# Kernel optimization log

Hardware: AMD Instinct MI355X
Metric: run time of the kernel (lower is better)

## Reference

```python
import jax, jax.numpy as jnp
import numpy as np

B, S, D, K = 4, 8192, 512, 20


def setup_inputs() -> dict:
    key = jax.random.key(0)
    k1, k2, k3, k4 = jax.random.split(key, 4)
    std = 0.02  # _init_weights: normal(0, 0.02/sqrt(layer_idx+1)), layer_idx=0
    return {
        "x": jax.random.normal(k1, (B, S, D), dtype=jnp.float32),
        "positions": jax.random.normal(k2, (K, D), dtype=jnp.float32) * 0.2,
        "log_scales": jnp.log(1.0 + 0.5 * jax.random.uniform(k3, (K,), dtype=jnp.float32)),
        "amplitudes": 1.2 + 0.3 * jax.random.uniform(k4, (K,), dtype=jnp.float32),
        "w_v": jax.random.normal(jax.random.fold_in(key, 10), (D, D), dtype=jnp.float32) * std,
        "w_o": jax.random.normal(jax.random.fold_in(key, 11), (D, D), dtype=jnp.float32) * std,
    }


def reference(x, positions, log_scales, amplitudes, w_v, w_o):
    # Gaussian-splat RBF attention (token -> splat -> token routing).
    scales = jnp.exp(log_scales)  # [K]
    # squared distances ||x - c||^2 via expansion (avoids [B,S,K,D] tensor)
    x2 = jnp.sum(x * x, axis=-1, keepdims=True)           # [B,S,1]
    c2 = jnp.sum(positions * positions, axis=-1)          # [K]
    xc = jnp.einsum('bsd,kd->bsk', x, positions)          # [B,S,K]
    d2 = jnp.maximum(x2 - 2.0 * xc + c2, 0.0)             # [B,S,K]
    gauss = amplitudes * jnp.exp(-0.5 * d2 / (scales * scales))  # [B,S,K]
    attn = gauss / (jnp.sum(gauss, axis=-1, keepdims=True) + 1e-8)  # per-token normalize
    v = jnp.einsum('bsd,ed->bse', x, w_v)                 # token_value_proj (no bias)
    splat_states = jnp.einsum('bsk,bsd->bkd', attn, v)    # gather token values at splats
    out = jnp.einsum('bsk,bkd->bsd', attn, splat_states)  # scatter back to tokens
    return jnp.einsum('bsd,ed->bse', out, w_o)            # output_proj (dropout=eval identity)
```

## Files before the change

### kernel.cpp

```cpp
#include <hip/hip_runtime.h>
#include <hip/hip_bf16.h>

#define BB 4
#define SS 8192
#define DD 512
#define KK 20
#define CHUNKS 64

__global__ void k0_params(const float* __restrict__ pos,
                          const float* __restrict__ log_scales,
                          const float* __restrict__ amps,
                          float* __restrict__ params) {
  int k = blockIdx.x;
  int lane = threadIdx.x;
  float acc = 0.f;
  for (int d = lane; d < DD; d += 64) { float p = pos[k * DD + d]; acc += p * p; }
#pragma unroll
  for (int off = 32; off > 0; off >>= 1) acc += __shfl_xor(acc, off);
  if (lane == 0) {
    params[k] = acc;
    float s = __expf(log_scales[k]);
    params[KK + k] = 0.5f / (s * s);
    params[2 * KK + k] = amps[k];
  }
}

__global__ __launch_bounds__(256) void k1_attn(
    const float* __restrict__ x, const float* __restrict__ pos,
    const float* __restrict__ params, float* __restrict__ attn) {
  __shared__ float pos_s[KK * DD];
  int tid = threadIdx.x;
  for (int i = tid; i < KK * DD / 4; i += 256)
    ((float4*)pos_s)[i] = ((const float4*)pos)[i];
  __syncthreads();

  int tl = tid >> 2;
  int dsub = tid & 3;
  size_t tok = (size_t)blockIdx.x * 64 + tl;
  const float* xrow = x + tok * DD;

  float acc[KK];
#pragma unroll
  for (int k = 0; k < KK; ++k) acc[k] = 0.f;
  float x2 = 0.f;

#pragma unroll 4
  for (int j = 0; j < 32; ++j) {
    int d0 = j * 16 + dsub * 4;
    float4 xv = *(const float4*)(xrow + d0);
    x2 += xv.x * xv.x + xv.y * xv.y + xv.z * xv.z + xv.w * xv.w;
#pragma unroll
    for (int k = 0; k < KK; ++k) {
      float4 p = *(const float4*)(pos_s + k * DD + d0);
      acc[k] += xv.x * p.x + xv.y * p.y + xv.z * p.z + xv.w * p.w;
    }
  }
#pragma unroll
  for (int k = 0; k < KK; ++k) {
    acc[k] += __shfl_xor(acc[k], 1);
    acc[k] += __shfl_xor(acc[k], 2);
  }
  x2 += __shfl_xor(x2, 1);
  x2 += __shfl_xor(x2, 2);

  if (dsub == 0) {
    float g[KK];
    float sum = 0.f;
#pragma unroll
    for (int k = 0; k < KK; ++k) {
      float d2 = fmaxf(x2 - 2.f * acc[k] + params[k], 0.f);
      float gk = params[2 * KK + k] * __expf(-params[KK + k] * d2);
      g[k] = gk;
      sum += gk;
    }
    float inv = 1.f / (sum + 1e-8f);
    float* arow = attn + tok * KK;
#pragma unroll
    for (int k = 0; k < KK; ++k) arow[k] = g[k] * inv;
  }
}

__global__ __launch_bounds__(256) void k2_scatter(
    const float* __restrict__ x, const float* __restrict__ attn,
    float* __restrict__ Mpart) {
  int t = threadIdx.x;
  int c = blockIdx.x;
  int b = blockIdx.y;
  int s0 = c * (SS / CHUNKS);

  float2 Ml[KK];
#pragma unroll
  for (int k = 0; k < KK; ++k) Ml[k] = make_float2(0.f, 0.f);

  for (int s = s0; s < s0 + SS / CHUNKS; ++s) {
    size_t tokb = (size_t)b * SS + s;
    float2 xv = *(const float2*)(x + tokb * DD + 2 * t);
    const float* arow = attn + tokb * KK;
#pragma unroll
    for (int k = 0; k < KK; ++k) {
      float a = arow[k];
      Ml[k].x += a * xv.x;
      Ml[k].y += a * xv.y;
    }
  }
  float* base = Mpart + (((size_t)b * CHUNKS + c) * KK) * DD + 2 * t;
#pragma unroll
  for (int k = 0; k < KK; ++k)
    *(float2*)(base + (size_t)k * DD) = Ml[k];
}

__global__ __launch_bounds__(256) void k2b_reduce(
    const float* __restrict__ Mpart, float* __restrict__ Mg) {
  int idx = blockIdx.x * 256 + threadIdx.x;
  int b = idx / (KK * DD);
  int kd = idx - b * (KK * DD);
  const float* p = Mpart + (size_t)b * CHUNKS * KK * DD + kd;
  float acc = 0.f;
#pragma unroll 8
  for (int c = 0; c < CHUNKS; ++c) acc += p[(size_t)c * KK * DD];
  Mg[idx] = acc;
}

__global__ __launch_bounds__(256) void k3_proj(
    const float* __restrict__ in, const float* __restrict__ W,
    float* __restrict__ out) {
  __shared__ float row_s[DD];
  int bk = blockIdx.x;
  int t = threadIdx.x;
  for (int i = t; i < DD / 4; i += 256)
    ((float4*)row_s)[i] = ((const float4*)(in + (size_t)bk * DD))[i];
  __syncthreads();
  int e = blockIdx.y * 256 + t;
  const float* wrow = W + (size_t)e * DD;
  float acc = 0.f;
#pragma unroll 4
  for (int j = 0; j < DD / 4; ++j) {
    float4 w4 = *(const float4*)(wrow + 4 * j);
    float4 m4 = ((const float4*)row_s)[j];
    acc += m4.x * w4.x + m4.y * w4.y + m4.z * w4.z + m4.w * w4.w;
  }
  out[(size_t)bk * DD + e] = acc;
}

__global__ __launch_bounds__(256) void k5_gather(
    const float* __restrict__ attn, const float* __restrict__ ws2,
    float* __restrict__ out) {
  int t = threadIdx.x;
  int b = blockIdx.y;
  int s0 = blockIdx.x * (SS / CHUNKS);

  float2 w[KK];
#pragma unroll
  for (int k = 0; k < KK; ++k)
    w[k] = *(const float2*)(ws2 + ((size_t)b * KK + k) * DD + 2 * t);

  for (int s = s0; s < s0 + SS / CHUNKS; ++s) {
    size_t tokb = (size_t)b * SS + s;
    const float* arow = attn + tokb * KK;
    float2 o = make_float2(0.f, 0.f);
#pragma unroll
    for (int k = 0; k < KK; ++k) {
      float a = arow[k];
      o.x += a * w[k].x;
      o.y += a * w[k].y;
    }
    *(float2*)(out + tokb * DD + 2 * t) = o;
  }
}

extern "C" void kernel_launch(void* const* d_in, const int* in_sizes, int n_in,
                              void* d_out, int out_size, void* d_ws, size_t ws_size,
                              hipStream_t stream) {
  const float* x   = (const float*)d_in[0];
  const float* pos = (const float*)d_in[1];
  const float* ls  = (const float*)d_in[2];
  const float* am  = (const float*)d_in[3];
  const float* w_v = (const float*)d_in[4];
  const float* w_o = (const float*)d_in[5];
  float* out = (float*)d_out;

  float* ws     = (float*)d_ws;
  float* params = ws;
  float* attn   = ws + 64;
  float* Mg     = attn + (size_t)BB * SS * KK;
  float* ssb    = Mg + (size_t)BB * KK * DD;
  float* ws2    = ssb + (size_t)BB * KK * DD;
  float* Mpart  = ws2 + (size_t)BB * KK * DD;

  k0_params<<<KK, 64, 0, stream>>>(pos, ls, am, params);
  k1_attn<<<(BB * SS) / 64, 256, 0, stream>>>(x, pos, params, attn);
  k2_scatter<<<dim3(CHUNKS, BB), 256, 0, stream>>>(x, attn, Mpart);
  k2b_reduce<<<(BB * KK * DD) / 256, 256, 0, stream>>>(Mpart, Mg);
  k3_proj<<<dim3(BB * KK, 2), 256, 0, stream>>>(Mg, w_v, ssb);
  k3_proj<<<dim3(BB * KK, 2), 256, 0, stream>>>(ssb, w_o, ws2);
  k5_gather<<<dim3(CHUNKS, BB), 256, 0, stream>>>(attn, ws2, out);
}
```

Before: 250.6 us.

## Restructure splat attention kernels for more parallelism and fuse reduce with projections

Rewrites the attention kernel so each block handles 32 tokens, with two rows per 16-lane group. Positions are reused across both rows and the params are cached in shared memory. The scatter stage runs on many more chunks (256 per batch, or 128 if the workspace is too small) and reads attention rows as float4. The chunk reduction and both projections are fused into one 512-thread kernel. The gather stage uses float4 outputs across 2048 blocks. The aim is to raise occupancy on the bandwidth-bound scatter/gather stages and cut launches. The cost is a larger partial-sum buffer and a serial 256-way reduction inside the fused kernel.

Result: slower. 280.8 us (+12.0%).

```diff
diff --git a/kernel.cpp b/kernel.cpp
--- a/kernel.cpp
+++ b/kernel.cpp
@@ -5,7 +5,10 @@
 #define SS 8192
 #define DD 512
 #define KK 20
-#define CHUNKS 64
+
+__device__ __forceinline__ float dot4(float4 a, float4 b) {
+  return a.x * b.x + a.y * b.y + a.z * b.z + a.w * b.w;
+}
 
 __global__ void k0_params(const float* __restrict__ pos,
                           const float* __restrict__ log_scales,
@@ -25,146 +28,180 @@
   }
 }
 
-__global__ __launch_bounds__(256) void k1_attn(
+__global__ __launch_bounds__(256) void kA_attn(
     const float* __restrict__ x, const float* __restrict__ pos,
-    const float* __restrict__ params, float* __restrict__ attn) {
+    const float* __restrict__ params, float* __restrict__ attn_g) {
   __shared__ float pos_s[KK * DD];
+  __shared__ float prm_s[3 * KK];
   int tid = threadIdx.x;
   for (int i = tid; i < KK * DD / 4; i += 256)
     ((float4*)pos_s)[i] = ((const float4*)pos)[i];
+  if (tid < 3 * KK) prm_s[tid] = params[tid];
   __syncthreads();
 
-  int tl = tid >> 2;
-  int dsub = tid & 3;
-  size_t tok = (size_t)blockIdx.x * 64 + tl;
-  const float* xrow = x + tok * DD;
-
-  float acc[KK];
-#pragma unroll
-  for (int k = 0; k < KK; ++k) acc[k] = 0.f;
-  float x2 = 0.f;
-
-#pragma unroll 4
-  for (int j = 0; j < 32; ++j) {
-    int d0 = j * 16 + dsub * 4;
-    float4 xv = *(const float4*)(xrow + d0);
-    x2 += xv.x * xv.x + xv.y * xv.y + xv.z * xv.z + xv.w * xv.w;
+  int b = blockIdx.x >> 8;
+  int c = blockIdx.x & 255;
+  size_t row0 = (size_t)b * SS + (size_t)c * 32;
+  int g = tid >> 4;
+  int dsub = tid & 15;
+
+  const float* xA = x + (row0 + g) * DD;
+  const float* xB = xA + 16 * DD;
+
+  float accA[KK], accB[KK], x2A = 0.f, x2B = 0.f;
+#pragma unroll
+  for (int k = 0; k < KK; ++k) { accA[k] = 0.f; accB[k] = 0.f; }
+
+#pragma unroll 2
+  for (int j = 0; j < 8; ++j) {
+    int d0 = j * 64 + dsub * 4;
+    float4 xa = *(const float4*)(xA + d0);
+    float4 xb = *(const float4*)(xB + d0);
+    x2A += dot4(xa, xa);
+    x2B += dot4(xb, xb);
 #pragma unroll
     for (int k = 0; k < KK; ++k) {
       float4 p = *(const float4*)(pos_s + k * DD + d0);
-      acc[k] += xv.x * p.x + xv.y * p.y + xv.z * p.z + xv.w * p.w;
-    }
-  }
+      accA[k] += dot4(xa, p);
+      accB[k] += dot4(xb, p);
+    }
+  }
+
+#pragma unroll
+  for (int m = 1; m <= 8; m <<= 1) { x2A += __shfl_xor(x2A, m); x2B += __shfl_xor(x2B, m); }
 #pragma unroll
   for (int k = 0; k < KK; ++k) {
-    acc[k] += __shfl_xor(acc[k], 1);
-    acc[k] += __shfl_xor(acc[k], 2);
-  }
-  x2 += __shfl_xor(x2, 1);
-  x2 += __shfl_xor(x2, 2);
+#pragma unroll
+    for (int m = 1; m <= 8; m <<= 1) {
+      accA[k] += __shfl_xor(accA[k], m);
+      accB[k] += __shfl_xor(accB[k], m);
+    }
+  }
 
   if (dsub == 0) {
-    float g[KK];
+    float gg[KK];
     float sum = 0.f;
 #pragma unroll
     for (int k = 0; k < KK; ++k) {
-      float d2 = fmaxf(x2 - 2.f * acc[k] + params[k], 0.f);
-      float gk = params[2 * KK + k] * __expf(-params[KK + k] * d2);
-      g[k] = gk;
-      sum += gk;
+      float d2 = fmaxf(x2A - 2.f * accA[k] + prm_s[k], 0.f);
+      gg[k] = prm_s[2 * KK + k] * __expf(-prm_s[KK + k] * d2);
+      sum += gg[k];
     }
     float inv = 1.f / (sum + 1e-8f);
-    float* arow = attn + tok * KK;
-#pragma unroll
-    for (int k = 0; k < KK; ++k) arow[k] = g[k] * inv;
-  }
-}
-
-__global__ __launch_bounds__(256) void k2_scatter(
+    float* ar = attn_g + (row0 + g) * KK;
+#pragma unroll
+    for (int k = 0; k < KK; ++k) ar[k] = gg[k] * inv;
+
+    sum = 0.f;
+#pragma unroll
+    for (int k = 0; k < KK; ++k) {
+      float d2 = fmaxf(x2B - 2.f * accB[k] + prm_s[k], 0.f);
+      gg[k] = prm_s[2 * KK + k] * __expf(-prm_s[KK + k] * d2);
+      sum += gg[k];
+    }
+    inv = 1.f / (sum + 1e-8f);
+    ar = attn_g + (row0 + g + 16) * KK;
+#pragma unroll
+    for (int k = 0; k < KK; ++k) ar[k] = gg[k] * inv;
+  }
+}
+
+__global__ __launch_bounds__(256) void kB_scatter(
     const float* __restrict__ x, const float* __restrict__ attn,
-    float* __restrict__ Mpart) {
+    float* __restrict__ Mpart, int tpc) {
   int t = threadIdx.x;
   int c = blockIdx.x;
   int b = blockIdx.y;
-  int s0 = c * (SS / CHUNKS);
+  int cpb = gridDim.x;
+  size_t row0 = (size_t)b * SS + (size_t)c * tpc;
 
   float2 Ml[KK];
 #pragma unroll
   for (int k = 0; k < KK; ++k) Ml[k] = make_float2(0.f, 0.f);
 
-  for (int s = s0; s < s0 + SS / CHUNKS; ++s) {
-    size_t tokb = (size_t)b * SS + s;
-    float2 xv = *(const float2*)(x + tokb * DD + 2 * t);
-    const float* arow = attn + tokb * KK;
-#pragma unroll
-    for (int k = 0; k < KK; ++k) {
-      float a = arow[k];
-      Ml[k].x += a * xv.x;
-      Ml[k].y += a * xv.y;
-    }
-  }
-  float* base = Mpart + (((size_t)b * CHUNKS + c) * KK) * DD + 2 * t;
-#pragma unroll
-  for (int k = 0; k < KK; ++k)
-    *(float2*)(base + (size_t)k * DD) = Ml[k];
-}
-
-__global__ __launch_bounds__(256) void k2b_reduce(
-    const float* __restrict__ Mpart, float* __restrict__ Mg) {
-  int idx = blockIdx.x * 256 + threadIdx.x;
-  int b = idx / (KK * DD);
-  int kd = idx - b * (KK * DD);
-  const float* p = Mpart + (size_t)b * CHUNKS * KK * DD + kd;
+  const float* xb = x + row0 * DD + 2 * t;
+  const float* ab = attn + row0 * KK;
+  for (int s = 0; s < tpc; ++s) {
+    float2 xv = *(const float2*)(xb + (size_t)s * DD);
+    const float4* ar4 = (const float4*)(ab + s * KK);
+#pragma unroll
+    for (int kk = 0; kk < KK / 4; ++kk) {
+      float4 a4 = ar4[kk];
+      Ml[4 * kk + 0].x += a4.x * xv.x; Ml[4 * kk + 0].y += a4.x * xv.y;
+      Ml[4 * kk + 1].x += a4.y * xv.x; Ml[4 * kk + 1].y += a4.y * xv.y;
+      Ml[4 * kk + 2].x += a4.z * xv.x; Ml[4 * kk + 2].y += a4.z * xv.y;
+      Ml[4 * kk + 3].x += a4.w * xv.x; Ml[4 * kk + 3].y += a4.w * xv.y;
+    }
+  }
+  float* mp = Mpart + ((size_t)b * cpb + c) * KK * DD + 2 * t;
+#pragma unroll
+  for (int k = 0; k < KK; ++k) *(float2*)(mp + (size_t)k * DD) = Ml[k];
+}
+
+__global__ __launch_bounds__(512) void k3f(
+    const float* __restrict__ Mpart, const float* __restrict__ w_v,
+    const float* __restrict__ w_o, float* __restrict__ ws2, int cpb) {
+  __shared__ float m_s[DD];
+  __shared__ float v_s[DD];
+  int bk = blockIdx.x;
+  int b = bk / KK, k = bk - b * KK;
+  int e = threadIdx.x;
+
+  const float* mp = Mpart + ((size_t)b * cpb) * KK * DD + (size_t)k * DD + e;
   float acc = 0.f;
 #pragma unroll 8
-  for (int c = 0; c < CHUNKS; ++c) acc += p[(size_t)c * KK * DD];
-  Mg[idx] = acc;
-}
-
-__global__ __launch_bounds__(256) void k3_proj(
-    const float* __restrict__ in, const float* __restrict__ W,
-    float* __restrict__ out) {
-  __shared__ float row_s[DD];
-  int bk = blockIdx.x;
-  int t = threadIdx.x;
-  for (int i = t; i < DD / 4; i += 256)
-    ((float4*)row_s)[i] = ((const float4*)(in + (size_t)bk * DD))[i];
+  for (int c = 0; c < cpb; ++c) acc += mp[(size_t)c * KK * DD];
+  m_s[e] = acc;
   __syncthreads();
-  int e = blockIdx.y * 256 + t;
-  const float* wrow = W + (size_t)e * DD;
-  float acc = 0.f;
+
+  const float4* wr = (const float4*)(w_v + (size_t)e * DD);
+  float a2 = 0.f;
 #pragma unroll 4
-  for (int j = 0; j < DD / 4; ++j) {
-    float4 w4 = *(const float4*)(wrow + 4 * j);
-    float4 m4 = ((const float4*)row_s)[j];
-    acc += m4.x * w4.x + m4.y * w4.y + m4.z * w4.z + m4.w * w4.w;
-  }
-  out[(size_t)bk * DD + e] = acc;
+  for (int j = 0; j < DD / 4; ++j) a2 += dot4(((const float4*)m_s)[j], wr[j]);
+  v_s[e] = a2;
+  __syncthreads();
+
+  const float4* wr2 = (const float4*)(w_o + (size_t)e * DD);
+  float a3 = 0.f;
+#pragma unroll 4
+  for (int j = 0; j < DD / 4; ++j) a3 += dot4(((const float4*)v_s)[j], wr2[j]);
+  ws2[(size_t)bk * DD + e] = a3;
 }
 
 __global__ __launch_bounds__(256) void k5_gather(
     const float* __restrict__ attn, const float* __restrict__ ws2,
     float* __restrict__ out) {
-  int t = threadIdx.x;
-  int b = blockIdx.y;
-  int s0 = blockIdx.x * (SS / CHUNKS);
-
-  float2 w[KK];
-#pragma unroll
-  for (int k = 0; k < KK; ++k)
-    w[k] = *(const float2*)(ws2 + ((size_t)b * KK + k) * DD + 2 * t);
-
-  for (int s = s0; s < s0 + SS / CHUNKS; ++s) {
-    size_t tokb = (size_t)b * SS + s;
-    const float* arow = attn + tokb * KK;
-    float2 o = make_float2(0.f, 0.f);
-#pragma unroll
-    for (int k = 0; k < KK; ++k) {
-      float a = arow[k];
-      o.x += a * w[k].x;
-      o.y += a * w[k].y;
-    }
-    *(float2*)(out + tokb * DD + 2 * t) = o;
+  int tid = threadIdx.x;
+  int b = blockIdx.x >> 9;
+  int sc = blockIdx.x & 511;
+  size_t s0 = (size_t)sc * 16;
+  int tr = tid >> 7;
+  int e4 = tid & 127;
+
+  float4 w[KK];
+  const float* wb = ws2 + (size_t)b * KK * DD + e4 * 4;
+#pragma unroll
+  for (int k = 0; k < KK; ++k) w[k] = *(const float4*)(wb + (size_t)k * DD);
+
+  size_t rowA = (size_t)b * SS + s0 + tr;
+  const float* ar = attn + rowA * KK;
+  float* orow = out + rowA * DD + e4 * 4;
+
+#pragma unroll 2
+  for (int i = 0; i < 8; ++i) {
+    const float4* a4 = (const float4*)(ar + (size_t)2 * i * KK);
+    float4 A = a4[0], Bv = a4[1], C = a4[2], Dv = a4[3], E = a4[4];
+    float4 o = make_float4(0.f, 0.f, 0.f, 0.f);
+#define ACC(av, kbase) \
+    o.x += av * w[kbase].x; o.y += av * w[kbase].y; \
+    o.z += av * w[kbase].z; o.w += av * w[kbase].w;
+    ACC(A.x, 0)  ACC(A.y, 1)  ACC(A.z, 2)  ACC(A.w, 3)
+    ACC(Bv.x, 4) ACC(Bv.y, 5) ACC(Bv.z, 6) ACC(Bv.w, 7)
+    ACC(C.x, 8)  ACC(C.y, 9)  ACC(C.z, 10) ACC(C.w, 11)
+    ACC(Dv.x, 12) ACC(Dv.y, 13) ACC(Dv.z, 14) ACC(Dv.w, 15)
+    ACC(E.x, 16) ACC(E.y, 17) ACC(E.z, 18) ACC(E.w, 19)
+#undef ACC
+    *(float4*)(orow + (size_t)2 * i * DD) = o;
   }
 }
 
@@ -180,18 +217,19 @@
   float* out = (float*)d_out;
 
   float* ws     = (float*)d_ws;
-  float* params = ws;
-  float* attn   = ws + 64;
-  float* Mg     = attn + (size_t)BB * SS * KK;
-  float* ssb    = Mg + (size_t)BB * KK * DD;
-  float* ws2    = ssb + (size_t)BB * KK * DD;
-  float* Mpart  = ws2 + (size_t)BB * KK * DD;
+  float* attn   = ws;
+  float* ws2    = attn + (size_t)BB * SS * KK;
+  float* params = ws2 + (size_t)BB * KK * DD;
+  float* Mpart  = params + 64;
+
+  size_t head_f = (size_t)BB * SS * KK + (size_t)BB * KK * DD + 64;
+  int cpb = 256, tpc = 32;
+  size_t need = (head_f + (size_t)BB * cpb * KK * DD) * sizeof(float);
+  if (ws_size < need) { cpb = 128; tpc = 64; }
 
   k0_params<<<KK, 64, 0, stream>>>(pos, ls, am, params);
-  k1_attn<<<(BB * SS) / 64, 256, 0, stream>>>(x, pos, params, attn);
-  k2_scatter<<<dim3(CHUNKS, BB), 256, 0, stream>>>(x, attn, Mpart);
-  k2b_reduce<<<(BB * KK * DD) / 256, 256, 0, stream>>>(Mpart, Mg);
-  k3_proj<<<dim3(BB * KK, 2), 256, 0, stream>>>(Mg, w_v, ssb);
-  k3_proj<<<dim3(BB * KK, 2), 256, 0, stream>>>(ssb, w_o, ws2);
-  k5_gather<<<dim3(CHUNKS, BB), 256, 0, stream>>>(attn, ws2, out);
-}
+  kA_attn<<<1024, 256, 0, stream>>>(x, pos, params, attn);
+  kB_scatter<<<dim3(cpb, BB), 256, 0, stream>>>(x, attn, Mpart, tpc);
+  k3f<<<BB * KK, 512, 0, stream>>>(Mpart, w_v, w_o, ws2, cpb);
+  k5_gather<<<2048, 256, 0, stream>>>(attn, ws2, out);
+}
```
